# Kernel tuning notes

Hardware: AMD Instinct MI355X
Metric: run time of the kernel (lower is better)

## Reference

```python
import jax, jax.numpy as jnp
import numpy as np


def setup_inputs() -> dict:
    key = jax.random.key(0)
    B = 4_000_000
    x = jax.random.normal(key, (B, 6), dtype=jnp.float32)
    return {"x": x}


def reference(x):
    # x: [B, 6] -> first 3 = so3 rotation vector w, last 3 = translation t.
    # expm of the skew-symmetric matrix K(w) equals Rodrigues' formula exactly:
    #   R = I + sin(theta)/theta * K + (1-cos(theta))/theta^2 * K^2,  theta = ||w||
    w = x[:, :3]
    t = x[:, 3:6]
    wx, wy, wz = w[:, 0], w[:, 1], w[:, 2]
    z = jnp.zeros_like(wx)
    # K = sum_i gen_i * w_i  (same generators as the TF layer)
    K = jnp.stack([
        jnp.stack([z, -wz, wy], axis=-1),
        jnp.stack([wz, z, -wx], axis=-1),
        jnp.stack([-wy, wx, z], axis=-1),
    ], axis=-2)  # [B, 3, 3]
    theta2 = jnp.sum(w * w, axis=-1)  # [B]
    small = theta2 < 1e-8
    theta = jnp.sqrt(jnp.where(small, 1.0, theta2))  # safe sqrt for grads
    # Taylor fallback near theta=0 to keep values/grads finite
    A = jnp.where(small, 1.0 - theta2 / 6.0, jnp.sin(theta) / theta)
    Bc = jnp.where(small, 0.5 - theta2 / 24.0, (1.0 - jnp.cos(theta)) / theta2)
    K2 = jnp.einsum('bij,bjk->bik', K, K)
    I = jnp.eye(3, dtype=x.dtype)
    R = I + A[:, None, None] * K + Bc[:, None, None] * K2  # [B, 3, 3]
    mat3x4 = jnp.concatenate([R, t[:, :, None]], axis=2)  # [B, 3, 4]
    last_row = jnp.broadcast_to(
        jnp.array([[[0.0, 0.0, 0.0, 1.0]]], dtype=x.dtype), (x.shape[0], 1, 4))
    return jnp.concatenate([mat3x4, last_row], axis=1)  # [B, 4, 4]
```

## Files before the change

### kernel.cpp

```cpp
#include <hip/hip_runtime.h>


#define TPB 256
#define P4 258

__global__ void __launch_bounds__(TPB)
so3_to_mat_kernel(const float* __restrict__ x, float* __restrict__ out, int n) {
    __shared__ float4 buf[4 * P4];
    const int t = threadIdx.x;
    const int ntiles = (n + TPB - 1) / TPB;

    for (int tile = blockIdx.x; tile < ntiles; tile += gridDim.x) {
        const int base = tile * TPB;
        const int row = base + t;

        if (row < n) {
            const float2* xr = reinterpret_cast<const float2*>(x) + 3 * (size_t)row;
            const float2 p0 = xr[0];
            const float2 p1 = xr[1];
            const float2 p2 = xr[2];
            const float wx = p0.x, wy = p0.y, wz = p1.x;
            const float tx = p1.y, ty = p2.x, tz = p2.y;

            const float t2 = wx * wx + wy * wy + wz * wz;
            const bool small = t2 < 1e-8f;

            const float th = sqrtf(small ? 1.0f : t2);
            float s, c;
            sincosf(th, &s, &c);
            const float A  = small ? (1.0f - t2 * (1.0f / 6.0f))  : (s / th);
            const float Bc = small ? (0.5f - t2 * (1.0f / 24.0f)) : ((1.0f - c) / t2);

            const float xx = wx * wx, yy = wy * wy, zz = wz * wz;
            const float xy = wx * wy, xz = wx * wz, yz = wy * wz;

            buf[0 * P4 + t] = make_float4(1.0f - Bc * (yy + zz),
                                          -A * wz + Bc * xy,
                                           A * wy + Bc * xz,
                                          tx);
            buf[1 * P4 + t] = make_float4( A * wz + Bc * xy,
                                          1.0f - Bc * (xx + zz),
                                          -A * wx + Bc * yz,
                                          ty);
            buf[2 * P4 + t] = make_float4(-A * wy + Bc * xz,
                                           A * wx + Bc * yz,
                                          1.0f - Bc * (xx + yy),
                                          tz);
            buf[3 * P4 + t] = make_float4(0.0f, 0.0f, 0.0f, 1.0f);
        }
        __syncthreads();

        const int nrow = min(TPB, n - base);
        float4* ob = reinterpret_cast<float4*>(out) + 4 * (size_t)base;
        #pragma unroll
        for (int m = 0; m < 4; ++m) {
            const int g = t + TPB * m;
            if (g < 4 * nrow) {
                const int r = g >> 2;
                const int s4 = g & 3;
                ob[g] = buf[s4 * P4 + r];
            }
        }
        __syncthreads();
    }
}

extern "C" void kernel_launch(void* const* d_in, const int* in_sizes, int n_in,
                              void* d_out, int out_size, void* d_ws, size_t ws_size,
                              hipStream_t stream) {
    const float* x = (const float*)d_in[0];
    float* out = (float*)d_out;
    const int n = in_sizes[0] / 6;

    const int ntiles = (n + TPB - 1) / TPB;
    int grid = ntiles < 2048 ? ntiles : 2048;

    so3_to_mat_kernel<<<grid, TPB, 0, stream>>>(x, out, n);
}
```

Before: 68.68 us.

## Prefetch next tile's input into registers and use lightweight LDS barriers

Loads each thread's input for the next grid-stride tile into registers before the store phase, so global load latency overlaps with the LDS transpose and output writes. It replaces __syncthreads with raw s_barrier plus an explicit LDS-only waitcnt, which avoids waiting on outstanding global loads. It also adds a fast path with no bounds checks for full tiles. The cost is more register pressure, and the hand-written barriers depend on correct memory ordering.

After: 69.55 us. About the same (+1.3%).

```diff
diff --git a/kernel.cpp b/kernel.cpp
--- a/kernel.cpp
+++ b/kernel.cpp
@@ -9,18 +9,27 @@
     __shared__ float4 buf[4 * P4];
     const int t = threadIdx.x;
     const int ntiles = (n + TPB - 1) / TPB;
+    const int tstride = gridDim.x;
 
-    for (int tile = blockIdx.x; tile < ntiles; tile += gridDim.x) {
+    int tile = blockIdx.x;
+    if (tile >= ntiles) return;
+
+    float2 q0 = make_float2(0.f, 0.f), q1 = q0, q2 = q0;
+    {
+        const int row = tile * TPB + t;
+        if (row < n) {
+            const float2* xr = reinterpret_cast<const float2*>(x) + 3 * (size_t)row;
+            q0 = xr[0]; q1 = xr[1]; q2 = xr[2];
+        }
+    }
+
+    for (; tile < ntiles; tile += tstride) {
         const int base = tile * TPB;
         const int row = base + t;
 
         if (row < n) {
-            const float2* xr = reinterpret_cast<const float2*>(x) + 3 * (size_t)row;
-            const float2 p0 = xr[0];
-            const float2 p1 = xr[1];
-            const float2 p2 = xr[2];
-            const float wx = p0.x, wy = p0.y, wz = p1.x;
-            const float tx = p1.y, ty = p2.x, tz = p2.y;
+            const float wx = q0.x, wy = q0.y, wz = q1.x;
+            const float tx = q1.y, ty = q2.x, tz = q2.y;
 
             const float t2 = wx * wx + wy * wy + wz * wz;
             const bool small = t2 < 1e-8f;
@@ -48,20 +57,41 @@
                                           tz);
             buf[3 * P4 + t] = make_float4(0.0f, 0.0f, 0.0f, 1.0f);
         }
-        __syncthreads();
+
+        {
+            const int nxt = tile + tstride;
+            if (nxt < ntiles) {
+                const int row2 = nxt * TPB + t;
+                if (row2 < n) {
+                    const float2* xr2 = reinterpret_cast<const float2*>(x) + 3 * (size_t)row2;
+                    q0 = xr2[0]; q1 = xr2[1]; q2 = xr2[2];
+                }
+            }
+        }
+
+        asm volatile("s_waitcnt lgkmcnt(0)" ::: "memory");
+        __builtin_amdgcn_s_barrier();
+        asm volatile("" ::: "memory");
 
         const int nrow = min(TPB, n - base);
         float4* ob = reinterpret_cast<float4*>(out) + 4 * (size_t)base;
-        #pragma unroll
-        for (int m = 0; m < 4; ++m) {
-            const int g = t + TPB * m;
-            if (g < 4 * nrow) {
-                const int r = g >> 2;
-                const int s4 = g & 3;
-                ob[g] = buf[s4 * P4 + r];
+        if (nrow == TPB) {
+            #pragma unroll
+            for (int m = 0; m < 4; ++m) {
+                const int g = t + TPB * m;
+                ob[g] = buf[(g & 3) * P4 + (g >> 2)];
+            }
+        } else {
+            #pragma unroll
+            for (int m = 0; m < 4; ++m) {
+                const int g = t + TPB * m;
+                if (g < 4 * nrow) ob[g] = buf[(g & 3) * P4 + (g >> 2)];
             }
         }
-        __syncthreads();
+
+        asm volatile("" ::: "memory");
+        __builtin_amdgcn_s_barrier();
+        asm volatile("" ::: "memory");
     }
 }
 
```
